# Optimization experiments

Measured on AMD Instinct MI355X. Metric: run time of the kernel, lower is better.

Reference implementation:

```python
import jax, jax.numpy as jnp
import numpy as np

E, H, F, N, B = 512, 8, 2048, 1024, 4
HD = E // H


def setup_inputs() -> dict:
    key = jax.random.key(0)
    ks = jax.random.split(key, 20)
    s = 0.02
    return {
        "node_inputs": jax.random.normal(ks[0], (N, B, E), jnp.float32),
        "parent_mask": jax.random.uniform(ks[1], (B, N, N), jnp.float32),
        "hidden": jax.random.bernoulli(ks[2], 0.5, (B, N, N)),
        "pad_mask": jax.random.bernoulli(ks[3], 0.1, (B, N)),
        "Wp": jax.random.normal(ks[4], (H, E), jnp.float32) * s,
        "bp": jnp.zeros((H,), jnp.float32),
        "Wc": jax.random.normal(ks[5], (H, E), jnp.float32) * s,
        "bc": jnp.zeros((H,), jnp.float32),
        "Wqkv": jax.random.normal(ks[6], (3 * E, E), jnp.float32) * s,
        "bqkv": jnp.zeros((3 * E,), jnp.float32),
        "Wo": jax.random.normal(ks[7], (E, E), jnp.float32) * s,
        "bo": jnp.zeros((E,), jnp.float32),
        "W1": jax.random.normal(ks[8], (F, E), jnp.float32) * s,
        "b1": jnp.zeros((F,), jnp.float32),
        "W2": jax.random.normal(ks[9], (E, F), jnp.float32) * s,
        "b2": jnp.zeros((E,), jnp.float32),
        "ln1_g": jnp.ones((E,), jnp.float32),
        "ln1_b": jnp.zeros((E,), jnp.float32),
        "ln2_g": jnp.ones((E,), jnp.float32),
        "ln2_b": jnp.zeros((E,), jnp.float32),
    }


def _layer_norm(x, g, b, eps=1e-5):
    m = jnp.mean(x, axis=-1, keepdims=True)
    v = jnp.mean((x - m) ** 2, axis=-1, keepdims=True)
    return (x - m) * jax.lax.rsqrt(v + eps) * g + b


def reference(node_inputs, parent_mask, hidden, pad_mask, Wp, bp, Wc, bc,
              Wqkv, bqkv, Wo, bo, W1, b1, W2, b2, ln1_g, ln1_b, ln2_g, ln2_b):
    x = node_inputs  # (N, B, E), seq-first like nn.TransformerEncoderLayer
    # parent/child per-head biases: Linear(E->H), permuted to (B, H, N)
    pbias = jnp.transpose(x @ Wp.T + bp, (1, 2, 0))
    cbias = jnp.transpose(x @ Wc.T + bc, (1, 2, 0))
    # additive attention bias (B, H, N, N)
    am = (jnp.swapaxes(parent_mask, 1, 2)[:, None] * pbias[..., None]
          + parent_mask[:, None] * cbias[..., None])
    am = jnp.where(hidden[:, None], -jnp.inf, am)
    # multi-head self-attention
    qkv = x @ Wqkv.T + bqkv  # (N, B, 3E)
    q, k, v = jnp.split(qkv, 3, axis=-1)

    def heads(t):  # (N, B, E) -> (B, H, N, HD)
        return jnp.transpose(t.reshape(N, B, H, HD), (1, 2, 0, 3))

    q, k, v = heads(q), heads(k), heads(v)
    scores = jnp.einsum("bhqd,bhkd->bhqk", q, k) / jnp.sqrt(jnp.float32(HD)) + am
    scores = jnp.where(pad_mask[:, None, None, :], -jnp.inf, scores)
    attn = jax.nn.softmax(scores, axis=-1)
    ctx = jnp.einsum("bhqk,bhkd->bhqd", attn, v)  # (B, H, N, HD)
    ctx = jnp.transpose(ctx, (2, 0, 1, 3)).reshape(N, B, E)
    attn_out = ctx @ Wo.T + bo
    # post-norm transformer encoder layer (dropout=0, relu activation)
    y = _layer_norm(x + attn_out, ln1_g, ln1_b)
    ff = jax.nn.relu(y @ W1.T + b1) @ W2.T + b2
    return _layer_norm(y + ff, ln2_g, ln2_b)
```

## Files before the change

### kernel.cpp

```cpp
#include <hip/hip_runtime.h>
#include <hip/hip_bf16.h>
#include <stdint.h>

using bf16 = __hip_bfloat16;

typedef __bf16 bf16x8 __attribute__((ext_vector_type(8)));
typedef float  f32x4  __attribute__((ext_vector_type(4)));

__device__ __forceinline__ float bflo(uint32_t u) { return __uint_as_float(u << 16); }
__device__ __forceinline__ float bfhi(uint32_t u) { return __uint_as_float(u & 0xffff0000u); }

__device__ __forceinline__ void load8(const bf16* p, float* f) {
  uint4 u = *(const uint4*)p;
  f[0] = bflo(u.x); f[1] = bfhi(u.x);
  f[2] = bflo(u.y); f[3] = bfhi(u.y);
  f[4] = bflo(u.z); f[5] = bfhi(u.z);
  f[6] = bflo(u.w); f[7] = bfhi(u.w);
}
__device__ __forceinline__ void load8(const float* p, float* f) {
  float4 a = *(const float4*)p, b = *(const float4*)(p + 4);
  f[0] = a.x; f[1] = a.y; f[2] = a.z; f[3] = a.w;
  f[4] = b.x; f[5] = b.y; f[6] = b.z; f[7] = b.w;
}
__device__ __forceinline__ void store1(float* o, float v) { *o = v; }
__device__ __forceinline__ void store1(bf16* o, float v) { *o = __float2bfloat16(v); }
__device__ __forceinline__ uint32_t bfbits(float x) {
  bf16 v = __float2bfloat16(x);
  return (uint32_t)*(uint16_t*)&v;
}

typedef const uint32_t __attribute__((address_space(1)))* gp_t;
typedef uint32_t __attribute__((address_space(3)))* lp_t;
__device__ __forceinline__ void gload16(const void* g, void* l) {
  __builtin_amdgcn_global_load_lds((gp_t)g, (lp_t)l, 16, 0, 0);
}

__global__ __launch_bounds__(256)
void prologue(const float* __restrict__ pm, const int* __restrict__ hid,
              const int* __restrict__ padm, uint32_t* __restrict__ mout,
              const float* __restrict__ x, const float* __restrict__ Wqkv,
              const float* __restrict__ Wo, const float* __restrict__ W1,
              const float* __restrict__ W2, bf16* __restrict__ xb,
              bf16* __restrict__ wq, bf16* __restrict__ wob,
              bf16* __restrict__ w1b, bf16* __restrict__ w2b,
              const float* __restrict__ bqkv, const float* __restrict__ bp,
              const float* __restrict__ bc, const float* __restrict__ Wp,
              const float* __restrict__ Wc, float* __restrict__ bias_ext)
{
  __shared__ float tileT[128][65];
  const int blk = blockIdx.x, t = threadIdx.x;
  if (blk < 512) {
    const int k0 = (blk & 7) * 128, q0 = ((blk >> 3) & 15) * 64, b = blk >> 7;
    const size_t pb = (size_t)b << 20;
#pragma unroll
    for (int i = 0; i < 32; ++i) {
      int idx = t + i * 256;
      int r = idx >> 6, c = idx & 63;
      tileT[r][c] = pm[pb + (size_t)(k0 + r) * 1024 + q0 + c];
    }
    __syncthreads();
#pragma unroll
    for (int i = 0; i < 32; ++i) {
      int idx = t + i * 256;
      int q = idx >> 7, k = idx & 127;
      size_t src = pb + (size_t)(q0 + q) * 1024 + k0 + k;
      int msk = hid[src] | padm[b * 1024 + k0 + k];
      uint32_t u = 0xFFFFFFFFu;
      if (!msk) u = (bfbits(tileT[k][q]) << 16) | bfbits(pm[src]);
      mout[src] = u;
    }
  } else if (blk < 3072) {
    size_t j = ((size_t)(blk - 512) * 256 + t) * 8;
    const float* s; bf16* o; size_t off;
    if      (j < 2097152) { s = x;    o = xb;  off = j; }
    else if (j < 2883584) { s = Wqkv; o = wq;  off = j - 2097152; }
    else if (j < 3145728) { s = Wo;   o = wob; off = j - 2883584; }
    else if (j < 4194304) { s = W1;   o = w1b; off = j - 3145728; }
    else                  { s = W2;   o = w2b; off = j - 4194304; }
    float f[8];
    load8(s + off, f);
    uint4 u;
    u.x = (bfbits(f[1]) << 16) | bfbits(f[0]);
    u.y = (bfbits(f[3]) << 16) | bfbits(f[2]);
    u.z = (bfbits(f[5]) << 16) | bfbits(f[4]);
    u.w = (bfbits(f[7]) << 16) | bfbits(f[6]);
    *(uint4*)(o + off) = u;
  } else {
    int sb = blk - 3072;
    if (sb < 2) {
      int j = (sb * 256 + t) * 8;
      if (j < 4096) {
        float f[8]; load8(Wp + j, f);
#pragma unroll
        for (int i = 0; i < 8; ++i) wq[(size_t)1536 * 512 + j + i] = __float2bfloat16(f[i]);
      }
    } else if (sb < 4) {
      int j = ((sb - 2) * 256 + t) * 8;
      if (j < 4096) {
        float f[8]; load8(Wc + j, f);
#pragma unroll
        for (int i = 0; i < 8; ++i) wq[(size_t)1544 * 512 + j + i] = __float2bfloat16(f[i]);
      }
    } else {
      int j = t * 8;
#pragma unroll
      for (int i = 0; i < 8; ++i) {
        int cc = j + i;
        if (cc < 1664) {
          float v = 0.f;
          if (cc < 1536) v = bqkv[cc];
          else if (cc < 1544) v = bp[cc - 1536];
          else if (cc < 1552) v = bc[cc - 1544];
          bias_ext[cc] = v;
        }
      }
    }
  }
}

template<int MODE, int BN>
__global__ __launch_bounds__(256)
void gemm_bt(const bf16* __restrict__ A, const bf16* __restrict__ W,
             const float* __restrict__ bias, bf16* __restrict__ outb,
             float* __restrict__ outf, int M, int Nout, int K, int kLen)
{
  constexpr int NT = BN / 32;
  __shared__ bf16 As[128 * 64];
  __shared__ bf16 Bs[BN * 64];
  const int t = threadIdx.x, lane = t & 63, wave = t >> 6;
  const int m0 = blockIdx.y * 128, n0 = blockIdx.x * BN;
  const int kOff = blockIdx.z * kLen;
  if (MODE == 3) outf += (size_t)blockIdx.z * M * Nout;
  const int wr = wave >> 1, wc = wave & 1;
  const int frow = lane & 15, ksel = (lane >> 4) * 8;
  f32x4 acc[4 * NT] = {};
  const bf16* Ab = A + (size_t)m0 * K;
  const bf16* Wb = W + (size_t)n0 * K;

  for (int k0 = kOff; k0 < kOff + kLen; k0 += 64) {
    __syncthreads();
#pragma unroll
    for (int i = 0; i < 4; ++i) {
      int ib = i * 256 + wave * 64;
      int idx = ib + lane;
      gload16(Ab + (size_t)(idx >> 3) * K + k0 + (idx & 7) * 8, As + ib * 8);
    }
#pragma unroll
    for (int i = 0; i < BN / 32; ++i) {
      int ib = i * 256 + wave * 64;
      int idx = ib + lane;
      gload16(Wb + (size_t)(idx >> 3) * K + k0 + (idx & 7) * 8, Bs + ib * 8);
    }
    __syncthreads();
#pragma unroll
    for (int kk = 0; kk < 64; kk += 32) {
      bf16x8 af[4], bf_[NT];
#pragma unroll
      for (int mt = 0; mt < 4; ++mt)
        af[mt] = *(const bf16x8*)(As + (wr * 64 + mt * 16 + frow) * 64 + kk + ksel);
#pragma unroll
      for (int nt = 0; nt < NT; ++nt)
        bf_[nt] = *(const bf16x8*)(Bs + (wc * (BN / 2) + nt * 16 + frow) * 64 + kk + ksel);
#pragma unroll
      for (int mt = 0; mt < 4; ++mt)
#pragma unroll
        for (int nt = 0; nt < NT; ++nt)
          acc[mt * NT + nt] = __builtin_amdgcn_mfma_f32_16x16x32_bf16(
              af[mt], bf_[nt], acc[mt * NT + nt], 0, 0, 0);
    }
  }
  const int rb = (lane >> 4) * 4, cb = lane & 15;
#pragma unroll
  for (int mt = 0; mt < 4; ++mt)
#pragma unroll
    for (int nt = 0; nt < NT; ++nt) {
      f32x4 a = acc[mt * NT + nt];
#pragma unroll
      for (int r = 0; r < 4; ++r) {
        int row = m0 + wr * 64 + mt * 16 + rb + r;
        int col = n0 + wc * (BN / 2) + nt * 16 + cb;
        if (MODE == 3) {
          outf[(size_t)row * Nout + col] = a[r];
        } else {
          float v = a[r] + bias[col];
          if (MODE == 1) v = fmaxf(v, 0.f);
          if (MODE == 2) {
            if (col >= 1552) continue;
            int n = row >> 2, b = row & 3;
            if (col >= 1536) {
              int j = col - 1536;
              int hh = j & 7;
              outf[(j < 8 ? 0 : 32768) + (b * 8 + hh) * 1024 + n] = v;
            } else {
              int which = col >> 9, hh = (col >> 6) & 7, d = col & 63;
              if (which == 0) v *= 0.125f;
              size_t idx;
              if (which == 2)
                idx = (((size_t)(64 + b * 8 + hh)) << 16) + (size_t)d * 1024 + n;
              else
                idx = (((size_t)(which * 32 + b * 8 + hh)) << 16) + (size_t)n * 64 + d;
              outb[idx] = __float2bfloat16(v);
            }
          } else {
            outb[(size_t)row * Nout + col] = __float2bfloat16(v);
          }
        }
      }
    }
}

__global__ __launch_bounds__(256, 6)
void attn_mfma(const bf16* __restrict__ qkv, const float* __restrict__ pbw,
               const float* __restrict__ cbw, const uint32_t* __restrict__ mpk,
               bf16* __restrict__ ctxo)
{
  __shared__ bf16 Kt[64 * 64];
  __shared__ bf16 Vt[64 * 64];
  __shared__ bf16 Ps[4][16][72];
  const int t = threadIdx.x, lane = t & 63, wave = t >> 6;
  const int g = lane >> 4, c = lane & 15;
  const int h = blockIdx.y, b = blockIdx.z;
  const int q0 = blockIdx.x * 64 + wave * 16;
  const size_t bh = (size_t)b * 8 + h;
  const bf16* Qp = qkv + (bh << 16);
  const bf16* Kp = qkv + ((32 + bh) << 16);
  const bf16* Vg = qkv + ((64 + bh) << 16);

  bf16x8 qa0 = *(const bf16x8*)(Qp + (size_t)(q0 + c) * 64 + g * 8);
  bf16x8 qa1 = *(const bf16x8*)(Qp + (size_t)(q0 + c) * 64 + 32 + g * 8);

  const float pbq = pbw[bh * 1024 + q0 + c];
  const float cbq = cbw[bh * 1024 + q0 + c];
  const uint32_t* mrp = mpk + (((size_t)b * 1024 + q0 + c) << 10);

  f32x4 oacc[4] = {{0,0,0,0},{0,0,0,0},{0,0,0,0},{0,0,0,0}};
  float m = -1e30f, l = 0.f;

  for (int kt = 0; kt < 16; ++kt) {
    const int k0 = kt * 64;
    __syncthreads();
#pragma unroll
    for (int i = 0; i < 2; ++i) {
      int ib = i * 256 + wave * 64;
      int idx = ib + lane;
      int r = idx >> 3, p = idx & 7;
      gload16(Kp + (size_t)(k0 + r) * 64 + ((p ^ (r & 7)) * 8), Kt + ib * 8);
    }
#pragma unroll
    for (int i = 0; i < 2; ++i) {
      int ib = i * 256 + wave * 64;
      int idx = ib + lane;
      int d = idx >> 3, p = idx & 7;
      gload16(Vg + (size_t)d * 1024 + k0 + ((p ^ (d & 7)) * 8), Vt + ib * 8);
    }
    uint4 mu[4];
#pragma unroll
    for (int nt = 0; nt < 4; ++nt)
      mu[nt] = *(const uint4*)(mrp + k0 + nt * 16 + 4 * g);
    __syncthreads();
    f32x4 sacc[4];
#pragma unroll
    for (int nt = 0; nt < 4; ++nt) {
      f32x4 z = {0.f,0.f,0.f,0.f};
      int r = nt * 16 + c;
      bf16x8 k0f = *(const bf16x8*)(Kt + r * 64 + (( g      ^ (c & 7)) * 8));
      bf16x8 k1f = *(const bf16x8*)(Kt + r * 64 + (((4 + g) ^ (c & 7)) * 8));
      z = __builtin_amdgcn_mfma_f32_16x16x32_bf16(k0f, qa0, z, 0, 0, 0);
      z = __builtin_amdgcn_mfma_f32_16x16x32_bf16(k1f, qa1, z, 0, 0, 0);
      sacc[nt] = z;
    }
    float mx = -1e30f;
#pragma unroll
    for (int nt = 0; nt < 4; ++nt) {
      uint32_t uu[4] = {mu[nt].x, mu[nt].y, mu[nt].z, mu[nt].w};
#pragma unroll
      for (int r = 0; r < 4; ++r) {
        float s = sacc[nt][r] + bfhi(uu[r]) * pbq + bflo(uu[r]) * cbq;
        s = (uu[r] == 0xFFFFFFFFu) ? -1e30f : s;
        sacc[nt][r] = s;
        mx = fmaxf(mx, s);
      }
    }
    mx = fmaxf(mx, __shfl_xor(mx, 16));
    mx = fmaxf(mx, __shfl_xor(mx, 32));
    const float newm = fmaxf(m, mx);
    const float al = __expf(m - newm);
    float ps = 0.f;
#pragma unroll
    for (int nt = 0; nt < 4; ++nt) {
      float p0 = (sacc[nt][0] <= -1e29f) ? 0.f : __expf(sacc[nt][0] - newm);
      float p1 = (sacc[nt][1] <= -1e29f) ? 0.f : __expf(sacc[nt][1] - newm);
      float p2 = (sacc[nt][2] <= -1e29f) ? 0.f : __expf(sacc[nt][2] - newm);
      float p3 = (sacc[nt][3] <= -1e29f) ? 0.f : __expf(sacc[nt][3] - newm);
      ps += (p0 + p1) + (p2 + p3);
      uint2 w;
      w.x = (bfbits(p1) << 16) | bfbits(p0);
      w.y = (bfbits(p3) << 16) | bfbits(p2);
      *(uint2*)&Ps[wave][c][nt * 16 + 4 * g] = w;
    }
    ps += __shfl_xor(ps, 16);
    ps += __shfl_xor(ps, 32);
    l = l * al + ps;
    m = newm;
#pragma unroll
    for (int dt = 0; dt < 4; ++dt) {
      oacc[dt][0] *= al; oacc[dt][1] *= al;
      oacc[dt][2] *= al; oacc[dt][3] *= al;
    }
#pragma unroll
    for (int dt = 0; dt < 4; ++dt) {
      int row = dt * 16 + c;
#pragma unroll
      for (int kc = 0; kc < 2; ++kc) {
        bf16x8 vf = *(const bf16x8*)(Vt + row * 64 + (((kc * 4 + g) ^ (c & 7)) * 8));
        bf16x8 pf = *(const bf16x8*)&Ps[wave][c][kc * 32 + g * 8];
        oacc[dt] = __builtin_amdgcn_mfma_f32_16x16x32_bf16(vf, pf, oacc[dt], 0, 0, 0);
      }
    }
  }
  const float inv = (l > 0.f) ? 1.f / l : 0.f;
  const int qg = q0 + c;
#pragma unroll
  for (int dt = 0; dt < 4; ++dt)
#pragma unroll
    for (int rg = 0; rg < 4; ++rg) {
      int d = dt * 16 + 4 * g + rg;
      ctxo[((size_t)qg * 4 + b) * 512 + h * 64 + d] =
          __float2bfloat16(oacc[dt][rg] * inv);
    }
}

template<typename TA, typename TO>
__global__ __launch_bounds__(256)
void ln_res2(const TA* __restrict__ a, const float* __restrict__ p0,
             const float* __restrict__ p1, const float* __restrict__ bias,
             const float* __restrict__ g, const float* __restrict__ be,
             TO* __restrict__ out)
{
  const int wave = threadIdx.x >> 6, lane = threadIdx.x & 63;
  const int m = blockIdx.x * 4 + wave;
  const size_t base = (size_t)m * 512 + lane * 8;
  float va[8], f0[8], f1[8], bb[8];
  load8(a + base, va);
  load8(p0 + base, f0);
  load8(p1 + base, f1);
  load8(bias + lane * 8, bb);
  float v[8], s = 0.f;
#pragma unroll
  for (int j = 0; j < 8; ++j) { v[j] = va[j] + f0[j] + f1[j] + bb[j]; s += v[j]; }
#pragma unroll
  for (int off = 32; off; off >>= 1) s += __shfl_xor(s, off);
  const float mean = s * (1.f / 512.f);
  float q = 0.f;
#pragma unroll
  for (int j = 0; j < 8; ++j) { float d = v[j] - mean; q += d * d; }
#pragma unroll
  for (int off = 32; off; off >>= 1) q += __shfl_xor(q, off);
  const float rs = rsqrtf(q * (1.f / 512.f) + 1e-5f);
  float gv[8], bv[8];
  load8(g + lane * 8, gv);
  load8(be + lane * 8, bv);
#pragma unroll
  for (int j = 0; j < 8; ++j)
    store1(out + base + j, (v[j] - mean) * rs * gv[j] + bv[j]);
}

extern "C" void kernel_launch(void* const* d_in, const int* in_sizes, int n_in,
                              void* d_out, int out_size, void* d_ws, size_t ws_size,
                              hipStream_t stream)
{
  (void)in_sizes; (void)n_in; (void)out_size; (void)ws_size;
  const float* x    = (const float*)d_in[0];
  const float* pm   = (const float*)d_in[1];
  const int*   hid  = (const int*)d_in[2];
  const int*   padm = (const int*)d_in[3];
  const float* Wp   = (const float*)d_in[4];
  const float* bp   = (const float*)d_in[5];
  const float* Wc   = (const float*)d_in[6];
  const float* bc   = (const float*)d_in[7];
  const float* Wqkv = (const float*)d_in[8];
  const float* bqkv = (const float*)d_in[9];
  const float* Wo   = (const float*)d_in[10];
  const float* bo   = (const float*)d_in[11];
  const float* W1   = (const float*)d_in[12];
  const float* b1   = (const float*)d_in[13];
  const float* W2   = (const float*)d_in[14];
  const float* b2   = (const float*)d_in[15];
  const float* g1   = (const float*)d_in[16];
  const float* be1  = (const float*)d_in[17];
  const float* g2   = (const float*)d_in[18];
  const float* be2  = (const float*)d_in[19];

  char* ws = (char*)d_ws;
  bf16*     qkvb  = (bf16*)    (ws);
  float*    pbo   = (float*)   (ws + 12582912);
  float*    cbo   = (float*)   (ws + 12713984);
  uint32_t* mpk   = (uint32_t*)(ws + 12845056);
  bf16*     ctx   = (bf16*)    (ws + 29622272);
  float*    part  = (float*)   (ws);
  bf16*     ff1   = (bf16*)    (ws + 16777216);
  bf16*     y     = (bf16*)    (ws + 33816576);
  bf16*     xb    = (bf16*)    (ws + 38010880);
  bf16*     wqkvb = (bf16*)    (ws + 42205184);
  bf16*     wob   = (bf16*)    (ws + 43909120);
  bf16*     w1b   = (bf16*)    (ws + 44433408);
  bf16*     w2b   = (bf16*)    (ws + 46530560);
  float*    bext  = (float*)   (ws + 48627712);
  float*    part1 = part + (size_t)4096 * 512;

  prologue<<<3077, 256, 0, stream>>>(pm, hid, padm, mpk, x, Wqkv, Wo, W1, W2,
                                     xb, wqkvb, wob, w1b, w2b,
                                     bqkv, bp, bc, Wp, Wc, bext);
  gemm_bt<2, 128><<<dim3(13, 32), 256, 0, stream>>>(xb, wqkvb, bext, qkvb, pbo, 4096, 1664, 512, 512);
  attn_mfma<<<dim3(16, 8, 4), 256, 0, stream>>>(qkvb, pbo, cbo, mpk, ctx);
  gemm_bt<3, 64><<<dim3(8, 32, 2), 256, 0, stream>>>(ctx, wob, nullptr, nullptr, part, 4096, 512, 512, 256);
  ln_res2<float, bf16><<<1024, 256, 0, stream>>>(x, part, part1, bo, g1, be1, y);
  gemm_bt<1, 128><<<dim3(16, 32), 256, 0, stream>>>(y, w1b, b1, ff1, nullptr, 4096, 2048, 512, 512);
  gemm_bt<3, 64><<<dim3(8, 32, 2), 256, 0, stream>>>(ff1, w2b, nullptr, nullptr, part, 4096, 512, 2048, 1024);
  ln_res2<bf16, float><<<1024, 256, 0, stream>>>(y, part, part1, b2, g2, be2, (float*)d_out);
}
```

Measured before the change: 297.4 us.

## Split attention over key halves with a separate merge kernel and larger key tiles

The attention kernel now splits the key range into two halves across blocks, which doubles the grid from 512 to 1024 blocks. Each block handles its half with 128-key tiles instead of 64 and writes unnormalized partial outputs plus running max and sum. A new reduction kernel merges the two halves with log-sum-exp weighting and writes the normalized context. This adds parallelism and halves the number of loop iterations, at the cost of an extra launch, partial-output traffic, bf16 rounding of the unnormalized partials, and lower occupancy from more shared memory and registers.

```diff
diff --git a/kernel.cpp b/kernel.cpp
--- a/kernel.cpp
+++ b/kernel.cpp
@@ -209,17 +209,17 @@
     }
 }
 
-__global__ __launch_bounds__(256, 6)
+__global__ __launch_bounds__(256, 3)
 void attn_mfma(const bf16* __restrict__ qkv, const float* __restrict__ pbw,
                const float* __restrict__ cbw, const uint32_t* __restrict__ mpk,
-               bf16* __restrict__ ctxo)
-{
-  __shared__ bf16 Kt[64 * 64];
-  __shared__ bf16 Vt[64 * 64];
-  __shared__ bf16 Ps[4][16][72];
+               bf16* __restrict__ opart, float2* __restrict__ mlout)
+{
+  __shared__ bf16 Kt[128 * 64];
+  __shared__ bf16 Vt[64 * 128];
+  __shared__ bf16 Ps[4][16][136];
   const int t = threadIdx.x, lane = t & 63, wave = t >> 6;
   const int g = lane >> 4, c = lane & 15;
-  const int h = blockIdx.y, b = blockIdx.z;
+  const int h = blockIdx.y, b = blockIdx.z >> 1, half = blockIdx.z & 1;
   const int q0 = blockIdx.x * 64 + wave * 16;
   const size_t bh = (size_t)b * 8 + h;
   const bf16* Qp = qkv + (bh << 16);
@@ -236,31 +236,31 @@
   f32x4 oacc[4] = {{0,0,0,0},{0,0,0,0},{0,0,0,0},{0,0,0,0}};
   float m = -1e30f, l = 0.f;
 
-  for (int kt = 0; kt < 16; ++kt) {
-    const int k0 = kt * 64;
+  for (int kt = 0; kt < 4; ++kt) {
+    const int k0 = half * 512 + kt * 128;
     __syncthreads();
 #pragma unroll
-    for (int i = 0; i < 2; ++i) {
+    for (int i = 0; i < 4; ++i) {
       int ib = i * 256 + wave * 64;
       int idx = ib + lane;
       int r = idx >> 3, p = idx & 7;
       gload16(Kp + (size_t)(k0 + r) * 64 + ((p ^ (r & 7)) * 8), Kt + ib * 8);
     }
 #pragma unroll
-    for (int i = 0; i < 2; ++i) {
+    for (int i = 0; i < 4; ++i) {
       int ib = i * 256 + wave * 64;
       int idx = ib + lane;
-      int d = idx >> 3, p = idx & 7;
-      gload16(Vg + (size_t)d * 1024 + k0 + ((p ^ (d & 7)) * 8), Vt + ib * 8);
-    }
-    uint4 mu[4];
-#pragma unroll
-    for (int nt = 0; nt < 4; ++nt)
+      int d = idx >> 4, p = idx & 15;
+      gload16(Vg + (size_t)d * 1024 + k0 + ((p ^ (d & 15)) * 8), Vt + ib * 8);
+    }
+    uint4 mu[8];
+#pragma unroll
+    for (int nt = 0; nt < 8; ++nt)
       mu[nt] = *(const uint4*)(mrp + k0 + nt * 16 + 4 * g);
     __syncthreads();
-    f32x4 sacc[4];
-#pragma unroll
-    for (int nt = 0; nt < 4; ++nt) {
+    f32x4 sacc[8];
+#pragma unroll
+    for (int nt = 0; nt < 8; ++nt) {
       f32x4 z = {0.f,0.f,0.f,0.f};
       int r = nt * 16 + c;
       bf16x8 k0f = *(const bf16x8*)(Kt + r * 64 + (( g      ^ (c & 7)) * 8));
@@ -271,7 +271,7 @@
     }
     float mx = -1e30f;
 #pragma unroll
-    for (int nt = 0; nt < 4; ++nt) {
+    for (int nt = 0; nt < 8; ++nt) {
       uint32_t uu[4] = {mu[nt].x, mu[nt].y, mu[nt].z, mu[nt].w};
 #pragma unroll
       for (int r = 0; r < 4; ++r) {
@@ -287,7 +287,7 @@
     const float al = __expf(m - newm);
     float ps = 0.f;
 #pragma unroll
-    for (int nt = 0; nt < 4; ++nt) {
+    for (int nt = 0; nt < 8; ++nt) {
       float p0 = (sacc[nt][0] <= -1e29f) ? 0.f : __expf(sacc[nt][0] - newm);
       float p1 = (sacc[nt][1] <= -1e29f) ? 0.f : __expf(sacc[nt][1] - newm);
       float p2 = (sacc[nt][2] <= -1e29f) ? 0.f : __expf(sacc[nt][2] - newm);
@@ -311,23 +311,43 @@
     for (int dt = 0; dt < 4; ++dt) {
       int row = dt * 16 + c;
 #pragma unroll
-      for (int kc = 0; kc < 2; ++kc) {
-        bf16x8 vf = *(const bf16x8*)(Vt + row * 64 + (((kc * 4 + g) ^ (c & 7)) * 8));
+      for (int kc = 0; kc < 4; ++kc) {
+        bf16x8 vf = *(const bf16x8*)(Vt + row * 128 + (((kc * 4 + g) ^ c) * 8));
         bf16x8 pf = *(const bf16x8*)&Ps[wave][c][kc * 32 + g * 8];
         oacc[dt] = __builtin_amdgcn_mfma_f32_16x16x32_bf16(vf, pf, oacc[dt], 0, 0, 0);
       }
     }
   }
-  const float inv = (l > 0.f) ? 1.f / l : 0.f;
   const int qg = q0 + c;
+  const size_t prow = ((size_t)(half * 32) + bh) * 1024 + qg;
 #pragma unroll
   for (int dt = 0; dt < 4; ++dt)
 #pragma unroll
-    for (int rg = 0; rg < 4; ++rg) {
-      int d = dt * 16 + 4 * g + rg;
-      ctxo[((size_t)qg * 4 + b) * 512 + h * 64 + d] =
-          __float2bfloat16(oacc[dt][rg] * inv);
-    }
+    for (int rg = 0; rg < 4; ++rg)
+      opart[prow * 64 + dt * 16 + 4 * g + rg] = __float2bfloat16(oacc[dt][rg]);
+  if (g == 0) mlout[prow] = make_float2(m, l);
+}
+
+__global__ __launch_bounds__(256)
+void attn_reduce(const bf16* __restrict__ opart, const float2* __restrict__ ml,
+                 bf16* __restrict__ ctxo)
+{
+  const int idx = blockIdx.x * 256 + threadIdx.x;
+  const int row = idx >> 3, seg = (idx & 7) * 8;
+  float o0[8], o1[8];
+  load8(opart + (size_t)row * 64 + seg, o0);
+  load8(opart + (size_t)(row + 32768) * 64 + seg, o1);
+  const float2 ml0 = ml[row], ml1 = ml[row + 32768];
+  const float mst = fmaxf(ml0.x, ml1.x);
+  const float w0 = __expf(ml0.x - mst), w1 = __expf(ml1.x - mst);
+  const float denom = ml0.y * w0 + ml1.y * w1;
+  const float inv = (denom > 0.f) ? 1.f / denom : 0.f;
+  const int bh = row >> 10, q = row & 1023;
+  const int b = bh >> 3, h = bh & 7;
+  bf16* out = ctxo + ((size_t)q * 4 + b) * 512 + h * 64 + seg;
+#pragma unroll
+  for (int j = 0; j < 8; ++j)
+    out[j] = __float2bfloat16((o0[j] * w0 + o1[j] * w1) * inv);
 }
 
 template<typename TA, typename TO>
@@ -406,13 +426,16 @@
   bf16*     w1b   = (bf16*)    (ws + 44433408);
   bf16*     w2b   = (bf16*)    (ws + 46530560);
   float*    bext  = (float*)   (ws + 48627712);
+  bf16*     opart = (bf16*)    (ws + 48634368);
+  float2*   mlb   = (float2*)  (ws + 57022976);
   float*    part1 = part + (size_t)4096 * 512;
 
   prologue<<<3077, 256, 0, stream>>>(pm, hid, padm, mpk, x, Wqkv, Wo, W1, W2,
                                      xb, wqkvb, wob, w1b, w2b,
                                      bqkv, bp, bc, Wp, Wc, bext);
   gemm_bt<2, 128><<<dim3(13, 32), 256, 0, stream>>>(xb, wqkvb, bext, qkvb, pbo, 4096, 1664, 512, 512);
-  attn_mfma<<<dim3(16, 8, 4), 256, 0, stream>>>(qkvb, pbo, cbo, mpk, ctx);
+  attn_mfma<<<dim3(16, 8, 8), 256, 0, stream>>>(qkvb, pbo, cbo, mpk, opart, mlb);
+  attn_reduce<<<1024, 256, 0, stream>>>(opart, mlb, ctx);
   gemm_bt<3, 64><<<dim3(8, 32, 2), 256, 0, stream>>>(ctx, wob, nullptr, nullptr, part, 4096, 512, 512, 256);
   ln_res2<float, bf16><<<1024, 256, 0, stream>>>(x, part, part1, bo, g1, be1, y);
   gemm_bt<1, 128><<<dim3(16, 32), 256, 0, stream>>>(y, w1b, b1, ff1, nullptr, 4096, 2048, 512, 512);
```

After: 272.0 us. -8.5%, faster.
